# Kernel tuning notes

Hardware: AMD Instinct MI355X
Metric: run time of the kernel (lower is better)

## Reference

```python
import jax, jax.numpy as jnp
import numpy as np

V, MAXLEN, D, FF, H, L = 50257, 1024, 768, 3072, 12, 12
HD = D // H


def _ln(x, w, b, eps=1e-5):
    mu = jnp.mean(x, axis=-1, keepdims=True)
    var = jnp.var(x, axis=-1, keepdims=True)
    return (x - mu) * jax.lax.rsqrt(var + eps) * w + b


def setup_inputs() -> dict:
    key = jax.random.key(0)
    ks = jax.random.split(key, 16)
    s = 0.02
    inp = {
        "tokens": jax.random.randint(ks[0], (2, 1024), 0, V),
        "tok_embed": jax.random.normal(ks[1], (V, D), jnp.float32) * s,
        "pos_embed": jax.random.normal(ks[2], (MAXLEN, D), jnp.float32) * s,
        # stacked per-layer params, weights stored [in, out]
        "qkv_w": jax.random.normal(ks[3], (L, D, 3 * D), jnp.float32) * s,
        "qkv_b": jnp.zeros((L, 3 * D), jnp.float32),
        "proj_w": jax.random.normal(ks[4], (L, D, D), jnp.float32) * s,
        "proj_b": jnp.zeros((L, D), jnp.float32),
        "ln1_w": jnp.ones((L, D), jnp.float32),
        "ln1_b": jnp.zeros((L, D), jnp.float32),
        "ln2_w": jnp.ones((L, D), jnp.float32),
        "ln2_b": jnp.zeros((L, D), jnp.float32),
        "fc1_w": jax.random.normal(ks[5], (L, D, FF), jnp.float32) * s,
        "fc1_b": jnp.zeros((L, FF), jnp.float32),
        "fc2_w": jax.random.normal(ks[6], (L, FF, D), jnp.float32) * s,
        "fc2_b": jnp.zeros((L, D), jnp.float32),
        "lnf_w": jnp.ones((D,), jnp.float32),
        "lnf_b": jnp.zeros((D,), jnp.float32),
    }
    return inp


def _gpt2(tokens, tok_embed, pos_embed, qkv_w, qkv_b, proj_w, proj_b,
          ln1_w, ln1_b, ln2_w, ln2_b, fc1_w, fc1_b, fc2_w, fc2_b, lnf_w, lnf_b):
    B, T = tokens.shape
    x = tok_embed[tokens] + pos_embed[jnp.arange(T)][None, :, :]  # [B,T,D]
    causal = jnp.tril(jnp.ones((T, T), bool))[None, None]          # [1,1,T,T]
    neg = jnp.finfo(x.dtype).min

    def block(x, p):
        (qw, qb, pw, pb, l1w, l1b, l2w, l2b, f1w, f1b, f2w, f2b) = p
        h = _ln(x, l1w, l1b)
        qkv = h @ qw + qb                                          # [B,T,3D]
        q, k, v = jnp.split(qkv, 3, axis=-1)
        q = q.reshape(B, T, H, HD).transpose(0, 2, 1, 3)           # [B,H,T,HD]
        k = k.reshape(B, T, H, HD).transpose(0, 2, 1, 3)
        v = v.reshape(B, T, H, HD).transpose(0, 2, 1, 3)
        att = jnp.einsum('bhqd,bhkd->bhqk', q, k) / np.sqrt(HD).astype(x.dtype)
        att = jnp.where(causal, att, neg)
        att = jax.nn.softmax(att, axis=-1)
        o = jnp.einsum('bhqk,bhkd->bhqd', att, v)
        o = o.transpose(0, 2, 1, 3).reshape(B, T, D)
        x = x + o @ pw + pb
        h2 = _ln(x, l2w, l2b)
        ff = jax.nn.gelu(h2 @ f1w + f1b, approximate=True) @ f2w + f2b
        return x + ff, None

    params = (qkv_w, qkv_b, proj_w, proj_b, ln1_w, ln1_b, ln2_w, ln2_b,
              fc1_w, fc1_b, fc2_w, fc2_b)
    x, _ = jax.lax.scan(block, x, params)
    x = _ln(x, lnf_w, lnf_b)
    return x @ tok_embed.T                                         # tied lm_head [B,T,V]


def reference(tokens, tok_embed, pos_embed, qkv_w, qkv_b, proj_w, proj_b,
              ln1_w, ln1_b, ln2_w, ln2_b, fc1_w, fc1_b, fc2_w, fc2_b,
              lnf_w, lnf_b):
    return _gpt2(tokens, tok_embed, pos_embed, qkv_w, qkv_b, proj_w, proj_b,
                 ln1_w, ln1_b, ln2_w, ln2_b, fc1_w, fc1_b, fc2_w, fc2_b,
                 lnf_w, lnf_b)
```

## Files before the change

### kernel.cpp

```cpp
#include <hip/hip_runtime.h>

#define TT 1024
#define DD 768
#define FFD 3072
#define NH 12
#define NL 12
#define HDIM 64
#define VOC 50257
#define BT 2048

typedef __attribute__((ext_vector_type(8))) __bf16 bf16x8;
typedef __attribute__((ext_vector_type(4))) float f32x4;
typedef __attribute__((ext_vector_type(4))) unsigned short u16x4;
typedef unsigned short u16;

static __device__ __forceinline__ u16 f2bf(float f) {
  unsigned int u = __float_as_uint(f);
  u += 0x7FFF + ((u >> 16) & 1);
  return (u16)(u >> 16);
}

static __device__ __forceinline__ void load_lds16(const u16* g, u16* l) {
  __builtin_amdgcn_global_load_lds(
      (const __attribute__((address_space(1))) unsigned int*)g,
      (__attribute__((address_space(3))) unsigned int*)l, 16, 0, 0);
}

__global__ __launch_bounds__(256) void transpose_convert(
    const float* __restrict__ in, u16* __restrict__ out, int R, int C) {
  __shared__ float tile[32][33];
  const long long zo = (long long)blockIdx.z * R * C;
  const int c0 = blockIdx.x * 32, r0 = blockIdx.y * 32;
  const int tx = threadIdx.x & 31, ty = threadIdx.x >> 5;
#pragma unroll
  for (int i = 0; i < 32; i += 8)
    tile[ty + i][tx] = in[zo + (long long)(r0 + ty + i) * C + c0 + tx];
  __syncthreads();
#pragma unroll
  for (int i = 0; i < 32; i += 8)
    out[zo + (long long)(c0 + ty + i) * R + r0 + tx] = f2bf(tile[tx][ty + i]);
}

__global__ void convert_bf16(const float* __restrict__ in, u16* __restrict__ out,
                             long long n) {
  long long i = (long long)blockIdx.x * 256 + threadIdx.x;
  const long long stride = (long long)gridDim.x * 256;
  for (; i < n; i += stride) out[i] = f2bf(in[i]);
}

__global__ __launch_bounds__(256) void embed_kernel(
    const int* __restrict__ tokens, const float* __restrict__ tokE,
    const float* __restrict__ posE, float* __restrict__ x) {
  const int row = blockIdx.x;
  const int t = row & (TT - 1);
  const int tok = tokens[row];
  const int tid = threadIdx.x;
#pragma unroll
  for (int c = 0; c < 3; ++c) {
    int d = tid + c * 256;
    x[(long long)row * DD + d] = tokE[(long long)tok * DD + d] + posE[(long long)t * DD + d];
  }
}

__global__ __launch_bounds__(256) void layernorm_bf16(
    const float* __restrict__ x, const float* __restrict__ w,
    const float* __restrict__ b, u16* __restrict__ out) {
  const int row = blockIdx.x;
  const float* xr = x + (long long)row * DD;
  const int tid = threadIdx.x;
  float v[3];
  float s = 0.f, s2 = 0.f;
#pragma unroll
  for (int c = 0; c < 3; ++c) {
    float t = xr[tid + c * 256];
    v[c] = t; s += t; s2 += t * t;
  }
  for (int off = 32; off; off >>= 1) {
    s += __shfl_down(s, off, 64);
    s2 += __shfl_down(s2, off, 64);
  }
  __shared__ float rs[8];
  if ((tid & 63) == 0) { rs[tid >> 6] = s; rs[4 + (tid >> 6)] = s2; }
  __syncthreads();
  s = rs[0] + rs[1] + rs[2] + rs[3];
  s2 = rs[4] + rs[5] + rs[6] + rs[7];
  const float mu = s * (1.0f / DD);
  const float var = s2 * (1.0f / DD) - mu * mu;
  const float inv = rsqrtf(var + 1e-5f);
  u16* o = out + (long long)row * DD;
#pragma unroll
  for (int c = 0; c < 3; ++c) {
    int d = tid + c * 256;
    o[d] = f2bf((v[c] - mu) * inv * w[d] + b[d]);
  }
}

__global__ __launch_bounds__(256, 3) void flash_attn(
    const u16* __restrict__ qkv, const u16* __restrict__ vT,
    u16* __restrict__ attn) {
  __shared__ __align__(16) u16 Qs[64 * 64];
  __shared__ __align__(16) u16 Ks0[64 * 64];
  __shared__ __align__(16) u16 Ks1[64 * 64];
  __shared__ __align__(16) u16 Vs0[64 * 64];
  __shared__ __align__(16) u16 Vs1[64 * 64];
  __shared__ __align__(16) u16 Ps[4 * 16 * 72];

  const int id = blockIdx.x;
  const int qt = 15 - id / 24;
  const int z = id % 24;
  const int b = z / NH, h = z - (z / NH) * NH;
  const int q0 = qt * 64;

  const int tid = threadIdx.x;
  const int lane = tid & 63;
  const int wave = __builtin_amdgcn_readfirstlane(tid >> 6);
  const int mf = lane & 15;
  const int quad = lane >> 4;

  const int srow = wave * 16 + (lane >> 3);
  const int srow1 = srow + 8;
  const int sch0 = (((lane & 7) ^ ((srow >> 1) & 7))) * 8;
  const int sch1 = (((lane & 7) ^ ((srow1 >> 1) & 7))) * 8;
  const int lb = wave * 1024;

  const u16* qk_base = qkv + (long long)b * TT * 2304 + h * 64;

  auto stageKV = [&](u16* Kd, u16* Vd, int kv0) {
    load_lds16(qk_base + (long long)(kv0 + srow) * 2304 + 768 + sch0, Kd + lb);
    load_lds16(qk_base + (long long)(kv0 + srow1) * 2304 + 768 + sch1, Kd + lb + 512);
    load_lds16(vT + (long long)(z * 64 + srow) * 1024 + kv0 + sch0, Vd + lb);
    load_lds16(vT + (long long)(z * 64 + srow1) * 1024 + kv0 + sch1, Vd + lb + 512);
  };

  load_lds16(qk_base + (long long)(q0 + srow) * 2304 + sch0, Qs + lb);
  load_lds16(qk_base + (long long)(q0 + srow1) * 2304 + sch1, Qs + lb + 512);
  stageKV(Ks0, Vs0, 0);
  __syncthreads();

  bf16x8 qfr[2];
  {
    const int r = wave * 16 + mf;
    const int sw = (r >> 1) & 7;
#pragma unroll
    for (int ks = 0; ks < 2; ++ks)
      qfr[ks] = *(const bf16x8*)(Qs + r * 64 + (((ks * 4 + quad) ^ sw) * 8));
  }

  f32x4 oacc[4] = {};
  float mrun = -1e30f, lrun = 0.f;
  u16 *Kc = Ks0, *Vc = Vs0, *Kn = Ks1, *Vn = Vs1;

  for (int t = 0; t <= qt; ++t) {
    if (t < qt) stageKV(Kn, Vn, (t + 1) * 64);
    const int diag = (t == qt);

    f32x4 sacc[4] = {};
#pragma unroll
    for (int ks = 0; ks < 2; ++ks)
#pragma unroll
      for (int i = 0; i < 4; ++i) {
        const int r = i * 16 + mf;
        bf16x8 kfr = *(const bf16x8*)(Kc + r * 64 + (((ks * 4 + quad) ^ ((r >> 1) & 7)) * 8));
        sacc[i] = __builtin_amdgcn_mfma_f32_16x16x32_bf16(kfr, qfr[ks], sacc[i], 0, 0, 0);
      }

    float pv[4][4];
    float tmax = -1e30f;
#pragma unroll
    for (int i = 0; i < 4; ++i)
#pragma unroll
      for (int r = 0; r < 4; ++r) {
        float v = sacc[i][r] * 0.125f;
        if (diag) {
          const int kvl = i * 16 + quad * 4 + r;
          if (kvl > wave * 16 + mf) v = -1e30f;
        }
        pv[i][r] = v;
        tmax = fmaxf(tmax, v);
      }
    tmax = fmaxf(tmax, __shfl_xor(tmax, 16, 64));
    tmax = fmaxf(tmax, __shfl_xor(tmax, 32, 64));
    const float mnew = fmaxf(mrun, tmax);
    const float fac = __expf(mrun - mnew);
    float lsum = 0.f;
#pragma unroll
    for (int i = 0; i < 4; ++i)
#pragma unroll
      for (int r = 0; r < 4; ++r) {
        float e = __expf(pv[i][r] - mnew);
        pv[i][r] = e;
        lsum += e;
      }
    lsum += __shfl_xor(lsum, 16, 64);
    lsum += __shfl_xor(lsum, 32, 64);
    lrun = lrun * fac + lsum;
    mrun = mnew;

    float fo[4];
#pragma unroll
    for (int r = 0; r < 4; ++r) fo[r] = __shfl(fac, (lane & 48) | (quad * 4 + r), 64);
#pragma unroll
    for (int j = 0; j < 4; ++j)
#pragma unroll
      for (int r = 0; r < 4; ++r) oacc[j][r] *= fo[r];

#pragma unroll
    for (int i = 0; i < 4; ++i) {
      u16x4 pk;
#pragma unroll
      for (int r = 0; r < 4; ++r) pk[r] = f2bf(pv[i][r]);
      *(u16x4*)(Ps + wave * 1152 + mf * 72 + i * 16 + quad * 4) = pk;
    }
#pragma unroll
    for (int ks = 0; ks < 2; ++ks) {
      bf16x8 pfr = *(const bf16x8*)(Ps + wave * 1152 + mf * 72 + ks * 32 + quad * 8);
#pragma unroll
      for (int j = 0; j < 4; ++j) {
        const int r = j * 16 + mf;
        bf16x8 vfr = *(const bf16x8*)(Vc + r * 64 + (((ks * 4 + quad) ^ ((r >> 1) & 7)) * 8));
        oacc[j] = __builtin_amdgcn_mfma_f32_16x16x32_bf16(pfr, vfr, oacc[j], 0, 0, 0);
      }
    }
    __syncthreads();
    u16* tk = Kc; Kc = Kn; Kn = tk;
    u16* tv = Vc; Vc = Vn; Vn = tv;
  }

  const float linv = 1.0f / lrun;
  float li[4];
#pragma unroll
  for (int r = 0; r < 4; ++r) li[r] = __shfl(linv, (lane & 48) | (quad * 4 + r), 64);
#pragma unroll
  for (int j = 0; j < 4; ++j)
#pragma unroll
    for (int r = 0; r < 4; ++r) {
      const int q = q0 + wave * 16 + quad * 4 + r;
      const int d = j * 16 + mf;
      attn[(long long)(b * TT + q) * 768 + h * 64 + d] = f2bf(oacc[j][r] * li[r]);
    }
}

enum { EPI_F32 = 0, EPI_BF16_BIAS = 1, EPI_BF16_BIAS_GELU = 2, EPI_F32_BIAS_RES = 3,
       EPI_BF16 = 4, EPI_QKV = 5, EPI_SPLITK_RES = 6 };

template <int EPI>
__global__ __launch_bounds__(256, 3) void gemm_nt(
    const u16* __restrict__ A, const u16* __restrict__ Bm,
    const float* __restrict__ bias, const float* __restrict__ resid,
    void* __restrict__ Cout, u16* __restrict__ vtAux,
    int M, int N, int K, int lda, int ldb, int ldc,
    long long aHi, long long aLo, long long bHi, long long bLo,
    long long cHi, long long cLo, int Hdiv, int swapxy,
    int xcdChunk, int kSplit) {
  __shared__ __align__(16) u16 As0[128 * 32];
  __shared__ __align__(16) u16 As1[128 * 32];
  __shared__ __align__(16) u16 Bs0[128 * 32];
  __shared__ __align__(16) u16 Bs1[128 * 32];
  const int z = blockIdx.z;
  int zb = 0, zh = 0;
  long long koff = 0;
  if (kSplit > 1) {
    const int slice = K / kSplit;
    koff = (long long)z * slice;
    K = slice;
  } else {
    zb = z / Hdiv; zh = z - zb * Hdiv;
  }
  const u16* Ab = A + zb * aHi + zh * aLo + koff;
  const u16* Bb = Bm + zb * bHi + zh * bLo + koff;
  const long long cOff = (long long)zb * cHi + (long long)zh * cLo;

  int rx = blockIdx.x, ry = blockIdx.y;
  if (xcdChunk) {
    const int id = ry * gridDim.x + rx;
    const int w = (id & 7) * xcdChunk + (id >> 3);
    rx = w % gridDim.x;
    ry = w / gridDim.x;
  }
  const int bx = swapxy ? ry : rx;
  const int by = swapxy ? rx : ry;
  const int m0 = by * 128;
  const int n0 = bx * 128;

  const int tid = threadIdx.x;
  const int lane = tid & 63;
  const int wave = __builtin_amdgcn_readfirstlane(tid >> 6);
  const int wm = (wave >> 1) * 64;
  const int wn = (wave & 1) * 64;
  const int mf = lane & 15;
  const int quad = lane >> 4;

  const int sr0 = wave * 32 + (lane >> 2);
  const int sr1 = sr0 + 16;
  const int sc0 = ((lane & 3) ^ ((sr0 >> 1) & 3)) * 8;
  const int sc1 = ((lane & 3) ^ ((sr1 >> 1) & 3)) * 8;
  int br0 = n0 + sr0; if (br0 >= N) br0 = N - 1;
  int br1 = n0 + sr1; if (br1 >= N) br1 = N - 1;
  const u16* agp0 = Ab + (long long)(m0 + sr0) * lda + sc0;
  const u16* agp1 = Ab + (long long)(m0 + sr1) * lda + sc1;
  const u16* bgp0 = Bb + (long long)br0 * ldb + sc0;
  const u16* bgp1 = Bb + (long long)br1 * ldb + sc1;
  const int woff = wave * 1024;

  auto stage = [&](u16* Ad, u16* Bd, int kk) {
    load_lds16(agp0 + kk, Ad + woff);
    load_lds16(agp1 + kk, Ad + woff + 512);
    load_lds16(bgp0 + kk, Bd + woff);
    load_lds16(bgp1 + kk, Bd + woff + 512);
  };

  int aoff[4], boff[4];
#pragma unroll
  for (int i = 0; i < 4; ++i) {
    const int ar = wm + i * 16 + mf;
    aoff[i] = ar * 32 + ((quad ^ ((ar >> 1) & 3)) * 8);
    const int br = wn + i * 16 + mf;
    boff[i] = br * 32 + ((quad ^ ((br >> 1) & 3)) * 8);
  }

  f32x4 acc[4][4] = {};

  auto compute = [&](const u16* Asb, const u16* Bsb) {
    bf16x8 afr[4], bfr[4];
#pragma unroll
    for (int i = 0; i < 4; ++i) afr[i] = *(const bf16x8*)(Asb + aoff[i]);
#pragma unroll
    for (int j = 0; j < 4; ++j) bfr[j] = *(const bf16x8*)(Bsb + boff[j]);
#pragma unroll
    for (int i = 0; i < 4; ++i)
#pragma unroll
      for (int j = 0; j < 4; ++j)
        acc[i][j] = __builtin_amdgcn_mfma_f32_16x16x32_bf16(afr[i], bfr[j], acc[i][j], 0, 0, 0);
  };

  stage(As0, Bs0, 0);
  __syncthreads();
  for (int k0 = 0; k0 < K; k0 += 64) {
    if (k0 + 32 < K) stage(As1, Bs1, k0 + 32);
    compute(As0, Bs0);
    __syncthreads();
    if (k0 + 64 < K) stage(As0, Bs0, k0 + 64);
    compute(As1, Bs1);
    __syncthreads();
  }

#pragma unroll
  for (int j = 0; j < 4; ++j) {
    const int col = n0 + wn + j * 16 + mf;
    if (col >= N) continue;
    float bv = 0.0f;
    if (EPI == EPI_BF16_BIAS || EPI == EPI_BF16_BIAS_GELU || EPI == EPI_F32_BIAS_RES ||
        EPI == EPI_QKV)
      bv = bias[col];
    if (EPI == EPI_SPLITK_RES && z == 0) bv = bias[col];
    if (EPI == EPI_QKV && col >= 1536) {
      const int hd = col - 1536;
#pragma unroll
      for (int i = 0; i < 4; ++i) {
        const int t0 = m0 + wm + i * 16 + quad * 4;
        u16x4 pk;
#pragma unroll
        for (int r = 0; r < 4; ++r) pk[r] = f2bf(acc[i][j][r] + bv);
        const int b_ = t0 >> 10;
        const long long vi =
            ((long long)((b_ * NH + (hd >> 6)) * 64 + (hd & 63))) * 1024 + (t0 & 1023);
        *(u16x4*)(vtAux + vi) = pk;
      }
      continue;
    }
#pragma unroll
    for (int i = 0; i < 4; ++i) {
#pragma unroll
      for (int r = 0; r < 4; ++r) {
        const int row = m0 + wm + i * 16 + quad * 4 + r;
        float v = acc[i][j][r] + bv;
        if (EPI == EPI_BF16_BIAS_GELU) {
          float u = v + 0.044715f * v * v * v;
          v = 0.5f * v * (1.0f + tanhf(0.7978845608028654f * u));
        }
        const long long ci = cOff + (long long)row * ldc + col;
        if (EPI == EPI_SPLITK_RES) {
          atomicAdd((float*)Cout + ci, v);
        } else if (EPI == EPI_F32_BIAS_RES) {
          ((float*)Cout)[ci] = resid[(long long)row * ldc + col] + v;
        } else if (EPI == EPI_F32) {
          ((float*)Cout)[ci] = v;
        } else {
          ((u16*)Cout)[ci] = f2bf(v);
        }
      }
    }
  }
}

extern "C" void kernel_launch(void* const* d_in, const int* in_sizes, int n_in,
                              void* d_out, int out_size, void* d_ws, size_t ws_size,
                              hipStream_t stream) {
  const int* tokens      = (const int*)d_in[0];
  const float* tok_embed = (const float*)d_in[1];
  const float* pos_embed = (const float*)d_in[2];
  const float* qkv_w     = (const float*)d_in[3];
  const float* qkv_b     = (const float*)d_in[4];
  const float* proj_w    = (const float*)d_in[5];
  const float* proj_b    = (const float*)d_in[6];
  const float* ln1_w     = (const float*)d_in[7];
  const float* ln1_b     = (const float*)d_in[8];
  const float* ln2_w     = (const float*)d_in[9];
  const float* ln2_b     = (const float*)d_in[10];
  const float* fc1_w     = (const float*)d_in[11];
  const float* fc1_b     = (const float*)d_in[12];
  const float* fc2_w     = (const float*)d_in[13];
  const float* fc2_b     = (const float*)d_in[14];
  const float* lnf_w     = (const float*)d_in[15];
  const float* lnf_b     = (const float*)d_in[16];

  if (ws_size < 440u * 1024u * 1024u) return;

  char* p = (char*)d_ws;
  auto alloc = [&](size_t bytes) {
    void* r = (void*)p;
    p += (bytes + 255) & ~(size_t)255;
    return r;
  };
  u16* wq   = (u16*)alloc((size_t)NL * 2304 * 768 * 2);
  u16* wp   = (u16*)alloc((size_t)NL * 768 * 768 * 2);
  u16* w1   = (u16*)alloc((size_t)NL * 3072 * 768 * 2);
  u16* w2   = (u16*)alloc((size_t)NL * 768 * 3072 * 2);
  u16* te   = (u16*)alloc((size_t)VOC * 768 * 2);
  float* x  = (float*)alloc((size_t)BT * 768 * 4);
  u16* hbuf = (u16*)alloc((size_t)BT * 768 * 2);
  u16* qkv  = (u16*)alloc((size_t)BT * 2304 * 2);
  u16* vT   = (u16*)alloc((size_t)24 * 64 * 1024 * 2);
  u16* attn = (u16*)alloc((size_t)BT * 768 * 2);
  u16* ff   = (u16*)alloc((size_t)BT * 3072 * 2);
  u16* xf   = (u16*)alloc((size_t)BT * 768 * 2);

  transpose_convert<<<dim3(2304 / 32, 768 / 32, NL), 256, 0, stream>>>(qkv_w, wq, 768, 2304);
  transpose_convert<<<dim3(768 / 32, 768 / 32, NL), 256, 0, stream>>>(proj_w, wp, 768, 768);
  transpose_convert<<<dim3(3072 / 32, 768 / 32, NL), 256, 0, stream>>>(fc1_w, w1, 768, 3072);
  transpose_convert<<<dim3(768 / 32, 3072 / 32, NL), 256, 0, stream>>>(fc2_w, w2, 3072, 768);
  convert_bf16<<<4096, 256, 0, stream>>>(tok_embed, te, (long long)VOC * 768);
  embed_kernel<<<BT, 256, 0, stream>>>(tokens, tok_embed, pos_embed, x);

  for (int l = 0; l < NL; ++l) {
    layernorm_bf16<<<BT, 256, 0, stream>>>(x, ln1_w + l * 768, ln1_b + l * 768, hbuf);
    gemm_nt<EPI_QKV><<<dim3(2304 / 128, BT / 128, 1), 256, 0, stream>>>(
        hbuf, wq + (size_t)l * 2304 * 768, qkv_b + l * 2304, nullptr, qkv, vT,
        BT, 2304, 768, 768, 768, 2304, 0, 0, 0, 0, 0, 0, 1, 0, 288 / 8, 1);
    flash_attn<<<384, 256, 0, stream>>>(qkv, vT, attn);
    gemm_nt<EPI_SPLITK_RES><<<dim3(768 / 128, BT / 128, 2), 256, 0, stream>>>(
        attn, wp + (size_t)l * 768 * 768, proj_b + l * 768, nullptr, x, nullptr,
        BT, 768, 768, 768, 768, 768, 0, 0, 0, 0, 0, 0, 1, 0, 96 / 8, 2);
    layernorm_bf16<<<BT, 256, 0, stream>>>(x, ln2_w + l * 768, ln2_b + l * 768, hbuf);
    gemm_nt<EPI_BF16_BIAS_GELU><<<dim3(3072 / 128, BT / 128, 1), 256, 0, stream>>>(
        hbuf, w1 + (size_t)l * 3072 * 768, fc1_b + l * 3072, nullptr, ff, nullptr,
        BT, 3072, 768, 768, 768, 3072, 0, 0, 0, 0, 0, 0, 1, 0, 384 / 8, 1);
    gemm_nt<EPI_SPLITK_RES><<<dim3(768 / 128, BT / 128, 4), 256, 0, stream>>>(
        ff, w2 + (size_t)l * 768 * 3072, fc2_b + l * 768, nullptr, x, nullptr,
        BT, 768, 3072, 3072, 3072, 768, 0, 0, 0, 0, 0, 0, 1, 0, 96 / 8, 4);
  }
  layernorm_bf16<<<BT, 256, 0, stream>>>(x, lnf_w, lnf_b, xf);
  gemm_nt<EPI_F32><<<dim3(BT / 128, (VOC + 127) / 128, 1), 256, 0, stream>>>(
      xf, te, nullptr, nullptr, (float*)d_out, nullptr,
      BT, VOC, 768, 768, 768, VOC, 0, 0, 0, 0, 0, 0, 1, 1, 6288 / 8, 1);
}
```

Baseline: 2.580 ms.

## Replace split-K atomics with partial buffers reduced in layernorm; use 256-row lm_head tiles

The split-K projection and fc2 GEMMs now write plain fp32 partial tiles to a scratch buffer instead of doing atomicAdd into the residual. The following layernorm kernel sums those partials into the residual stream and then normalizes, so the reduction happens as part of a pass that already reads x. Separately, the GEMM is templated on the M tile size, and the large vocabulary projection now uses 256-row tiles, which halves the grid along M and reuses each loaded B tile across more rows. The cost is extra scratch traffic for the partials, and the larger tile drops the occupancy bound from 3 to 2 blocks.

```diff
diff --git a/kernel.cpp b/kernel.cpp
--- a/kernel.cpp
+++ b/kernel.cpp
@@ -62,17 +62,21 @@
   }
 }
 
-__global__ __launch_bounds__(256) void layernorm_bf16(
-    const float* __restrict__ x, const float* __restrict__ w,
-    const float* __restrict__ b, u16* __restrict__ out) {
+__global__ __launch_bounds__(256) void ln_sum(
+    float* __restrict__ x, const float* __restrict__ pp, int nsum,
+    const float* __restrict__ w, const float* __restrict__ b,
+    u16* __restrict__ out) {
   const int row = blockIdx.x;
-  const float* xr = x + (long long)row * DD;
+  const long long base = (long long)row * DD;
   const int tid = threadIdx.x;
   float v[3];
   float s = 0.f, s2 = 0.f;
 #pragma unroll
   for (int c = 0; c < 3; ++c) {
-    float t = xr[tid + c * 256];
+    const int d = tid + c * 256;
+    float t = x[base + d];
+    for (int q = 0; q < nsum; ++q) t += pp[(long long)q * BT * DD + base + d];
+    if (nsum) x[base + d] = t;
     v[c] = t; s += t; s2 += t * t;
   }
   for (int off = 32; off; off >>= 1) {
@@ -87,7 +91,7 @@
   const float mu = s * (1.0f / DD);
   const float var = s2 * (1.0f / DD) - mu * mu;
   const float inv = rsqrtf(var + 1e-5f);
-  u16* o = out + (long long)row * DD;
+  u16* o = out + base;
 #pragma unroll
   for (int c = 0; c < 3; ++c) {
     int d = tid + c * 256;
@@ -240,20 +244,22 @@
     }
 }
 
-enum { EPI_F32 = 0, EPI_BF16_BIAS = 1, EPI_BF16_BIAS_GELU = 2, EPI_F32_BIAS_RES = 3,
-       EPI_BF16 = 4, EPI_QKV = 5, EPI_SPLITK_RES = 6 };
-
-template <int EPI>
-__global__ __launch_bounds__(256, 3) void gemm_nt(
+enum { EPI_F32 = 0, EPI_BF16_BIAS = 1, EPI_BF16_BIAS_GELU = 2,
+       EPI_BF16 = 4, EPI_QKV = 5, EPI_SPLITK_PART = 6 };
+
+template <int EPI, int BM = 128>
+__global__ __launch_bounds__(256, BM == 256 ? 2 : 3) void gemm_nt(
     const u16* __restrict__ A, const u16* __restrict__ Bm,
-    const float* __restrict__ bias, const float* __restrict__ resid,
+    const float* __restrict__ bias,
     void* __restrict__ Cout, u16* __restrict__ vtAux,
     int M, int N, int K, int lda, int ldb, int ldc,
     long long aHi, long long aLo, long long bHi, long long bLo,
     long long cHi, long long cLo, int Hdiv, int swapxy,
     int xcdChunk, int kSplit) {
-  __shared__ __align__(16) u16 As0[128 * 32];
-  __shared__ __align__(16) u16 As1[128 * 32];
+  constexpr int AISS = BM / 64;
+  constexpr int MI = BM / 32;
+  __shared__ __align__(16) u16 As0[BM * 32];
+  __shared__ __align__(16) u16 As1[BM * 32];
   __shared__ __align__(16) u16 Bs0[128 * 32];
   __shared__ __align__(16) u16 Bs1[128 * 32];
   const int z = blockIdx.z;
@@ -279,55 +285,64 @@
   }
   const int bx = swapxy ? ry : rx;
   const int by = swapxy ? rx : ry;
-  const int m0 = by * 128;
+  const int m0 = by * BM;
   const int n0 = bx * 128;
 
   const int tid = threadIdx.x;
   const int lane = tid & 63;
   const int wave = __builtin_amdgcn_readfirstlane(tid >> 6);
-  const int wm = (wave >> 1) * 64;
+  const int wm = (wave >> 1) * (BM / 2);
   const int wn = (wave & 1) * 64;
   const int mf = lane & 15;
   const int quad = lane >> 4;
 
+  const u16* agp[AISS];
+#pragma unroll
+  for (int i = 0; i < AISS; ++i) {
+    const int r = wave * (BM / 4) + i * 16 + (lane >> 2);
+    const int c = ((lane & 3) ^ ((r >> 1) & 3)) * 8;
+    agp[i] = Ab + (long long)(m0 + r) * lda + c;
+  }
   const int sr0 = wave * 32 + (lane >> 2);
   const int sr1 = sr0 + 16;
   const int sc0 = ((lane & 3) ^ ((sr0 >> 1) & 3)) * 8;
   const int sc1 = ((lane & 3) ^ ((sr1 >> 1) & 3)) * 8;
   int br0 = n0 + sr0; if (br0 >= N) br0 = N - 1;
   int br1 = n0 + sr1; if (br1 >= N) br1 = N - 1;
-  const u16* agp0 = Ab + (long long)(m0 + sr0) * lda + sc0;
-  const u16* agp1 = Ab + (long long)(m0 + sr1) * lda + sc1;
   const u16* bgp0 = Bb + (long long)br0 * ldb + sc0;
   const u16* bgp1 = Bb + (long long)br1 * ldb + sc1;
+  const int aoffW = wave * (BM * 8);
   const int woff = wave * 1024;
 
   auto stage = [&](u16* Ad, u16* Bd, int kk) {
-    load_lds16(agp0 + kk, Ad + woff);
-    load_lds16(agp1 + kk, Ad + woff + 512);
+#pragma unroll
+    for (int i = 0; i < AISS; ++i) load_lds16(agp[i] + kk, Ad + aoffW + i * 512);
     load_lds16(bgp0 + kk, Bd + woff);
     load_lds16(bgp1 + kk, Bd + woff + 512);
   };
 
-  int aoff[4], boff[4];
-#pragma unroll
-  for (int i = 0; i < 4; ++i) {
+  int aoff[MI], boff[4];
+#pragma unroll
+  for (int i = 0; i < MI; ++i) {
     const int ar = wm + i * 16 + mf;
     aoff[i] = ar * 32 + ((quad ^ ((ar >> 1) & 3)) * 8);
-    const int br = wn + i * 16 + mf;
-    boff[i] = br * 32 + ((quad ^ ((br >> 1) & 3)) * 8);
-  }
-
-  f32x4 acc[4][4] = {};
+  }
+#pragma unroll
+  for (int j = 0; j < 4; ++j) {
+    const int br = wn + j * 16 + mf;
+    boff[j] = br * 32 + ((quad ^ ((br >> 1) & 3)) * 8);
+  }
+
+  f32x4 acc[MI][4] = {};
 
   auto compute = [&](const u16* Asb, const u16* Bsb) {
-    bf16x8 afr[4], bfr[4];
-#pragma unroll
-    for (int i = 0; i < 4; ++i) afr[i] = *(const bf16x8*)(Asb + aoff[i]);
+    bf16x8 afr[MI], bfr[4];
+#pragma unroll
+    for (int i = 0; i < MI; ++i) afr[i] = *(const bf16x8*)(Asb + aoff[i]);
 #pragma unroll
     for (int j = 0; j < 4; ++j) bfr[j] = *(const bf16x8*)(Bsb + boff[j]);
 #pragma unroll
-    for (int i = 0; i < 4; ++i)
+    for (int i = 0; i < MI; ++i)
 #pragma unroll
       for (int j = 0; j < 4; ++j)
         acc[i][j] = __builtin_amdgcn_mfma_f32_16x16x32_bf16(afr[i], bfr[j], acc[i][j], 0, 0, 0);
@@ -349,14 +364,13 @@
     const int col = n0 + wn + j * 16 + mf;
     if (col >= N) continue;
     float bv = 0.0f;
-    if (EPI == EPI_BF16_BIAS || EPI == EPI_BF16_BIAS_GELU || EPI == EPI_F32_BIAS_RES ||
-        EPI == EPI_QKV)
+    if (EPI == EPI_BF16_BIAS || EPI == EPI_BF16_BIAS_GELU || EPI == EPI_QKV)
       bv = bias[col];
-    if (EPI == EPI_SPLITK_RES && z == 0) bv = bias[col];
+    if (EPI == EPI_SPLITK_PART && z == 0) bv = bias[col];
     if (EPI == EPI_QKV && col >= 1536) {
       const int hd = col - 1536;
 #pragma unroll
-      for (int i = 0; i < 4; ++i) {
+      for (int i = 0; i < MI; ++i) {
         const int t0 = m0 + wm + i * 16 + quad * 4;
         u16x4 pk;
 #pragma unroll
@@ -369,7 +383,7 @@
       continue;
     }
 #pragma unroll
-    for (int i = 0; i < 4; ++i) {
+    for (int i = 0; i < MI; ++i) {
 #pragma unroll
       for (int r = 0; r < 4; ++r) {
         const int row = m0 + wm + i * 16 + quad * 4 + r;
@@ -378,15 +392,15 @@
           float u = v + 0.044715f * v * v * v;
           v = 0.5f * v * (1.0f + tanhf(0.7978845608028654f * u));
         }
-        const long long ci = cOff + (long long)row * ldc + col;
-        if (EPI == EPI_SPLITK_RES) {
-          atomicAdd((float*)Cout + ci, v);
-        } else if (EPI == EPI_F32_BIAS_RES) {
-          ((float*)Cout)[ci] = resid[(long long)row * ldc + col] + v;
-        } else if (EPI == EPI_F32) {
-          ((float*)Cout)[ci] = v;
+        if (EPI == EPI_SPLITK_PART) {
+          ((float*)Cout)[(long long)z * M * ldc + (long long)row * ldc + col] = v;
         } else {
-          ((u16*)Cout)[ci] = f2bf(v);
+          const long long ci = cOff + (long long)row * ldc + col;
+          if (EPI == EPI_F32) {
+            ((float*)Cout)[ci] = v;
+          } else {
+            ((u16*)Cout)[ci] = f2bf(v);
+          }
         }
       }
     }
@@ -434,6 +448,7 @@
   u16* attn = (u16*)alloc((size_t)BT * 768 * 2);
   u16* ff   = (u16*)alloc((size_t)BT * 3072 * 2);
   u16* xf   = (u16*)alloc((size_t)BT * 768 * 2);
+  float* pp = (float*)alloc((size_t)4 * BT * 768 * 4);
 
   transpose_convert<<<dim3(2304 / 32, 768 / 32, NL), 256, 0, stream>>>(qkv_w, wq, 768, 2304);
   transpose_convert<<<dim3(768 / 32, 768 / 32, NL), 256, 0, stream>>>(proj_w, wp, 768, 768);
@@ -443,24 +458,26 @@
   embed_kernel<<<BT, 256, 0, stream>>>(tokens, tok_embed, pos_embed, x);
 
   for (int l = 0; l < NL; ++l) {
-    layernorm_bf16<<<BT, 256, 0, stream>>>(x, ln1_w + l * 768, ln1_b + l * 768, hbuf);
+    ln_sum<<<BT, 256, 0, stream>>>(x, pp, l == 0 ? 0 : 4,
+                                   ln1_w + l * 768, ln1_b + l * 768, hbuf);
     gemm_nt<EPI_QKV><<<dim3(2304 / 128, BT / 128, 1), 256, 0, stream>>>(
-        hbuf, wq + (size_t)l * 2304 * 768, qkv_b + l * 2304, nullptr, qkv, vT,
+        hbuf, wq + (size_t)l * 2304 * 768, qkv_b + l * 2304, qkv, vT,
         BT, 2304, 768, 768, 768, 2304, 0, 0, 0, 0, 0, 0, 1, 0, 288 / 8, 1);
     flash_attn<<<384, 256, 0, stream>>>(qkv, vT, attn);
-    gemm_nt<EPI_SPLITK_RES><<<dim3(768 / 128, BT / 128, 2), 256, 0, stream>>>(
-        attn, wp + (size_t)l * 768 * 768, proj_b + l * 768, nullptr, x, nullptr,
+    gemm_nt<EPI_SPLITK_PART><<<dim3(768 / 128, BT / 128, 2), 256, 0, stream>>>(
+        attn, wp + (size_t)l * 768 * 768, proj_b + l * 768, pp, nullptr,
         BT, 768, 768, 768, 768, 768, 0, 0, 0, 0, 0, 0, 1, 0, 96 / 8, 2);
-    layernorm_bf16<<<BT, 256, 0, stream>>>(x, ln2_w + l * 768, ln2_b + l * 768, hbuf);
+    ln_sum<<<BT, 256, 0, stream>>>(x, pp, 2,
+                                   ln2_w + l * 768, ln2_b + l * 768, hbuf);
     gemm_nt<EPI_BF16_BIAS_GELU><<<dim3(3072 / 128, BT / 128, 1), 256, 0, stream>>>(
-        hbuf, w1 + (size_t)l * 3072 * 768, fc1_b + l * 3072, nullptr, ff, nullptr,
+        hbuf, w1 + (size_t)l * 3072 * 768, fc1_b + l * 3072, ff, nullptr,
         BT, 3072, 768, 768, 768, 3072, 0, 0, 0, 0, 0, 0, 1, 0, 384 / 8, 1);
-    gemm_nt<EPI_SPLITK_RES><<<dim3(768 / 128, BT / 128, 4), 256, 0, stream>>>(
-        ff, w2 + (size_t)l * 768 * 3072, fc2_b + l * 768, nullptr, x, nullptr,
+    gemm_nt<EPI_SPLITK_PART><<<dim3(768 / 128, BT / 128, 4), 256, 0, stream>>>(
+        ff, w2 + (size_t)l * 768 * 3072, fc2_b + l * 768, pp, nullptr,
         BT, 768, 3072, 3072, 3072, 768, 0, 0, 0, 0, 0, 0, 1, 0, 96 / 8, 4);
   }
-  layernorm_bf16<<<BT, 256, 0, stream>>>(x, lnf_w, lnf_b, xf);
-  gemm_nt<EPI_F32><<<dim3(BT / 128, (VOC + 127) / 128, 1), 256, 0, stream>>>(
-      xf, te, nullptr, nullptr, (float*)d_out, nullptr,
-      BT, VOC, 768, 768, 768, VOC, 0, 0, 0, 0, 0, 0, 1, 1, 6288 / 8, 1);
-}
+  ln_sum<<<BT, 256, 0, stream>>>(x, pp, 4, lnf_w, lnf_b, xf);
+  gemm_nt<EPI_F32, 256><<<dim3(BT / 256, (VOC + 127) / 128, 1), 256, 0, stream>>>(
+      xf, te, nullptr, (float*)d_out, nullptr,
+      BT, VOC, 768, 768, 768, VOC, 0, 0, 0, 0, 0, 0, 1, 1, 3144 / 8, 1);
+}
```

Measured after the change: 2.531 ms. No clear change (-1.9%).
